# Kernel optimization log

Hardware: AMD Instinct MI355X
Metric: run time of the kernel (lower is better)

## Reference

```python
import jax, jax.numpy as jnp
import numpy as np

# Dimensions: N sites, B batch, D bond dim, d physical dim, C output classes
N, B, D, d, C = 1024, 256, 16, 2, 10
STDDEV = 1e-5
INIT_DIAG = 1.0


def setup_inputs() -> dict:
    key = jax.random.key(0)
    k1, k2, k3 = jax.random.split(key, 3)
    x = jax.random.normal(k1, (N, B, d), dtype=jnp.float32)
    eye = jnp.eye(D, dtype=jnp.float32)
    # tensor[n,:,:,i] = init_diag * I + stddev * noise  (matches TF init)
    tensor = INIT_DIAG * eye[None, :, :, None] + STDDEV * jax.random.normal(k2, (N, D, D, d), dtype=jnp.float32)
    # Aout[c] = I + stddev * noise
    Aout = eye[None, :, :] + STDDEV * jax.random.normal(k3, (C, D, D), dtype=jnp.float32)
    return {"x": x, "tensor": tensor, "Aout": Aout}


def _chain_prod(A):
    # A: (n, b, D, D) -> ordered matrix-chain product (b, D, D), log-depth tree.
    # Faithful to parallel_contract: pairwise einsum per level; odd leftover is
    # kept at the end of the list (order-preserving, associativity-equivalent).
    while A.shape[0] > 1:
        n = A.shape[0]
        half = n // 2
        prod = jnp.einsum('nblk,nbkr->nblr', A[0:2 * half:2], A[1:2 * half:2])
        if n % 2 == 1:
            prod = jnp.concatenate([prod, A[-1:]], axis=0)
        A = prod
    return A[0]


def reference(x, tensor, Aout):
    # A: (N, B, D, D) site matrices after contracting input features
    A = jnp.einsum('nbi,nlri->nblr', x, tensor)
    nhalf = A.shape[0] // 2
    # Left half product, take row 0 (left boundary); right half, take col 0
    Al = _chain_prod(A[:nhalf])[:, 0, :]   # (B, D)
    Ar = _chain_prod(A[nhalf:])[:, :, 0]   # (B, D)
    # out[b,o] = Al[b] @ Aout[o] @ Ar[b]
    return jnp.einsum('bl,olr,br->bo', Al, Aout, Ar)
```

## Files before the change

### kernel.cpp

```cpp
#include <hip/hip_runtime.h>


#define BATCH  256
#define NCLS   10
#define NSITES 1024
#define NGRP   16
#define SEGLEN 16

typedef __attribute__((ext_vector_type(8))) short short8;
typedef __attribute__((ext_vector_type(4))) float f32x4;
typedef __attribute__((ext_vector_type(4))) unsigned short us4;

static __device__ __forceinline__ unsigned short bf16tr(float f) {
    return (unsigned short)(__builtin_bit_cast(unsigned, f) >> 16);
}
static __device__ __forceinline__ unsigned short bf16rne(float f) {
    unsigned u = __builtin_bit_cast(unsigned, f);
    u += 0x7FFFu + ((u >> 16) & 1u);
    return (unsigned short)(u >> 16);
}
static __device__ __forceinline__ float bf16tof(unsigned short h) {
    return __builtin_bit_cast(float, (unsigned)h << 16);
}

__global__ __launch_bounds__(256) void ta_pack_kernel(
    const float* __restrict__ tensor, unsigned short* __restrict__ Ta)
{
    __shared__ float s[512];
    const int n = blockIdx.x, t = threadIdx.x;
    *(float2*)(s + 2 * t) = *(const float2*)(tensor + (size_t)n * 512 + 2 * t);
    __syncthreads();
    const int o0 = 2 * t, m = o0 >> 5, k0 = o0 & 31;
    const float v0 = s[(k0 & 15) * 32 + m * 2 + (k0 >> 4)];
    const int k1 = k0 + 1;
    const float v1 = s[(k1 & 15) * 32 + m * 2 + (k1 >> 4)];
    const unsigned pk = (unsigned)bf16rne(v0) | ((unsigned)bf16rne(v1) << 16);
    ((unsigned*)Ta)[(size_t)n * 256 + t] = pk;
}

__global__ __launch_bounds__(256) void chain_kernel(
    const float* __restrict__ x,
    const unsigned short* __restrict__ Ta,
    unsigned short* __restrict__ M2)
{
    __shared__ unsigned short rm[4 * 256];
    __shared__ unsigned short cm[4 * 256];
    const int t = threadIdx.x, wave = t >> 6, lane = t & 63;
    const int quad = lane >> 4, l15 = lane & 15;
    const int b = blockIdx.x >> 4, g = blockIdx.x & 15;
    const int seg = g * 4 + wave, n0 = seg * SEGLEN;

    const int qm = quad & 1;
    const int bidx0 = (32 * qm + l15) * 4;
    const int bidx1 = bidx0 + 64;

    f32x4 d;
#pragma unroll
    for (int r = 0; r < 4; ++r) d[r] = (quad * 4 + r == l15) ? 1.0f : 0.0f;

    const float2* __restrict__ xp = (const float2*)x;

#pragma unroll 4
    for (int s = 0; s < SEGLEN; ++s) {
        const int n = n0 + s;
        const float2 xv = xp[(size_t)n * BATCH + b];
        const float xs = (quad < 2) ? xv.x : xv.y;
        const short8 af = *(const short8*)(Ta + (size_t)n * 512 + l15 * 32 + quad * 8);
        float w[8];
#pragma unroll
        for (int r = 0; r < 4; ++r) {
            w[r]     = __builtin_bit_cast(float,
                        __builtin_amdgcn_ds_bpermute(bidx0, __builtin_bit_cast(int, d[r])));
            w[4 + r] = __builtin_bit_cast(float,
                        __builtin_amdgcn_ds_bpermute(bidx1, __builtin_bit_cast(int, d[r])));
        }
        short8 bf;
#pragma unroll
        for (int j = 0; j < 8; ++j) bf[j] = (short)bf16tr(xs * w[j]);
        f32x4 c = {0.0f, 0.0f, 0.0f, 0.0f};
        d = __builtin_amdgcn_mfma_f32_16x16x32_bf16(af, bf, c, 0, 0, 0);
    }

#pragma unroll
    for (int r = 0; r < 4; ++r)
        rm[wave * 256 + (quad * 4 + r) * 16 + l15] = bf16tr(d[r]);
    {
        us4 pk = {bf16tr(d[0]), bf16tr(d[1]), bf16tr(d[2]), bf16tr(d[3])};
        *(us4*)(cm + wave * 256 + l15 * 16 + quad * 4) = pk;
    }
    __syncthreads();

    const short8 z8 = {0, 0, 0, 0, 0, 0, 0, 0};

    short8 af1 = z8, bf1 = z8;
    if (wave < 2 && quad < 2) {
        af1 = *(const short8*)(rm + (2 * wave + 1) * 256 + l15 * 16 + quad * 8);
        bf1 = *(const short8*)(cm + (2 * wave) * 256 + l15 * 16 + quad * 8);
    }
    __syncthreads();
    if (wave < 2) {
        f32x4 c = {0.0f, 0.0f, 0.0f, 0.0f};
        f32x4 q = __builtin_amdgcn_mfma_f32_16x16x32_bf16(af1, bf1, c, 0, 0, 0);
#pragma unroll
        for (int r = 0; r < 4; ++r)
            rm[wave * 256 + (quad * 4 + r) * 16 + l15] = bf16tr(q[r]);
        us4 pk = {bf16tr(q[0]), bf16tr(q[1]), bf16tr(q[2]), bf16tr(q[3])};
        *(us4*)(cm + wave * 256 + l15 * 16 + quad * 4) = pk;
    }
    __syncthreads();

    if (wave == 0) {
        short8 af2 = z8, bf2 = z8;
        if (quad < 2) {
            af2 = *(const short8*)(rm + 1 * 256 + l15 * 16 + quad * 8);
            bf2 = *(const short8*)(cm + 0 * 256 + l15 * 16 + quad * 8);
        }
        f32x4 c = {0.0f, 0.0f, 0.0f, 0.0f};
        f32x4 rr = __builtin_amdgcn_mfma_f32_16x16x32_bf16(af2, bf2, c, 0, 0, 0);
        us4 pk = {bf16tr(rr[0]), bf16tr(rr[1]), bf16tr(rr[2]), bf16tr(rr[3])};
        *(us4*)(M2 + ((size_t)b * NGRP + g) * 256 + l15 * 16 + quad * 4) = pk;
    }
}

__global__ __launch_bounds__(256) void combine_kernel(
    const unsigned short* __restrict__ M2,
    const float* __restrict__ Aout,
    float* __restrict__ out)
{
    __shared__ unsigned short rm[16 * 256];
    __shared__ unsigned short cm[16 * 256];
    const int b = blockIdx.x, t = threadIdx.x;
    const int wave = t >> 6, lane = t & 63, quad = lane >> 4, l15 = lane & 15;

    const short8* __restrict__ src = (const short8*)(M2 + (size_t)b * NGRP * 256);
#pragma unroll
    for (int i2 = 0; i2 < 2; ++i2) {
        const int i = t + 256 * i2;
        const short8 v = src[i];
        *((short8*)cm + i) = v;
        const int mat = i >> 5, c = (i >> 1) & 15, r0 = (i & 1) * 8;
#pragma unroll
        for (int e = 0; e < 8; ++e)
            rm[mat * 256 + (r0 + e) * 16 + c] = (unsigned short)v[e];
    }
    __syncthreads();

    const short8 z8 = {0, 0, 0, 0, 0, 0, 0, 0};

    for (int lvl = 0; lvl < 3; ++lvl) {
        const int np = 8 >> lvl;
        short8 afr[2], bfr[2];
        int pids[2], nmine = 0;
        for (int p = wave; p < np; p += 4) {
            short8 a = z8, bb = z8;
            if (quad < 2) {
                a  = *(const short8*)(rm + (2 * p + 1) * 256 + l15 * 16 + quad * 8);
                bb = *(const short8*)(cm + (2 * p) * 256 + l15 * 16 + quad * 8);
            }
            afr[nmine] = a; bfr[nmine] = bb; pids[nmine] = p; ++nmine;
        }
        __syncthreads();
        for (int ii = 0; ii < nmine; ++ii) {
            f32x4 c = {0.0f, 0.0f, 0.0f, 0.0f};
            f32x4 r = __builtin_amdgcn_mfma_f32_16x16x32_bf16(afr[ii], bfr[ii], c, 0, 0, 0);
            const int p = pids[ii];
#pragma unroll
            for (int rr = 0; rr < 4; ++rr)
                rm[p * 256 + (quad * 4 + rr) * 16 + l15] = bf16tr(r[rr]);
            us4 pk = {bf16tr(r[0]), bf16tr(r[1]), bf16tr(r[2]), bf16tr(r[3])};
            *(us4*)(cm + p * 256 + l15 * 16 + quad * 4) = pk;
        }
        __syncthreads();
    }

    if (t < NCLS * 16) {
        const int o = t >> 4, r = t & 15;
        const float vr = bf16tof(rm[256 + r]);
        float s = 0.0f;
#pragma unroll
        for (int l = 0; l < 16; ++l)
            s = __builtin_fmaf(bf16tof(rm[l * 16]), Aout[((size_t)o * 16 + l) * 16 + r], s);
        s *= vr;
#pragma unroll
        for (int off = 8; off > 0; off >>= 1)
            s += __shfl_xor(s, off, 16);
        if (r == 0) out[(size_t)b * NCLS + o] = s;
    }
}

extern "C" void kernel_launch(void* const* d_in, const int* in_sizes, int n_in,
                              void* d_out, int out_size, void* d_ws, size_t ws_size,
                              hipStream_t stream)
{
    const float* x      = (const float*)d_in[0];
    const float* tensor = (const float*)d_in[1];
    const float* Aout   = (const float*)d_in[2];
    float* out = (float*)d_out;

    unsigned short* Ta = (unsigned short*)d_ws;
    unsigned short* M2 = (unsigned short*)((char*)d_ws + (1 << 20));

    ta_pack_kernel<<<NSITES, 256, 0, stream>>>(tensor, Ta);
    chain_kernel<<<BATCH * NGRP, 256, 0, stream>>>(x, Ta, M2);
    combine_kernel<<<BATCH, 256, 0, stream>>>(M2, Aout, out);
}
```

Before: 89.16 us.

## Fuse chain and combine kernels into one per-batch 1024-thread block

Merges the segment-chain kernel and the combine kernel into one launch, with one 1024-thread block per batch element. Each of the 16 waves now advances four independent segment chains in an interleaved loop, giving the MFMA units independent work to hide latency. The full 64-matrix tree reduction then runs in shared memory, so the M2 round trip through global memory and one launch go away. The cost is only 256 blocks, which lowers the number of blocks in flight, plus higher register pressure from four accumulators per wave and 64 KB of LDS per block.

```diff
diff --git a/kernel.cpp b/kernel.cpp
--- a/kernel.cpp
+++ b/kernel.cpp
@@ -4,8 +4,10 @@
 #define BATCH  256
 #define NCLS   10
 #define NSITES 1024
-#define NGRP   16
+#define NSEGB  64
 #define SEGLEN 16
+#define NWAVE  16
+#define CPW    4
 
 typedef __attribute__((ext_vector_type(8))) short short8;
 typedef __attribute__((ext_vector_type(4))) float f32x4;
@@ -38,120 +40,72 @@
     ((unsigned*)Ta)[(size_t)n * 256 + t] = pk;
 }
 
-__global__ __launch_bounds__(256) void chain_kernel(
+__global__ __launch_bounds__(1024) void chain_kernel(
     const float* __restrict__ x,
     const unsigned short* __restrict__ Ta,
-    unsigned short* __restrict__ M2)
+    const float* __restrict__ Aout,
+    float* __restrict__ out)
 {
-    __shared__ unsigned short rm[4 * 256];
-    __shared__ unsigned short cm[4 * 256];
+    __shared__ unsigned short rm[NSEGB * 256];
+    __shared__ unsigned short cm[NSEGB * 256];
     const int t = threadIdx.x, wave = t >> 6, lane = t & 63;
     const int quad = lane >> 4, l15 = lane & 15;
-    const int b = blockIdx.x >> 4, g = blockIdx.x & 15;
-    const int seg = g * 4 + wave, n0 = seg * SEGLEN;
+    const int b = blockIdx.x;
 
     const int qm = quad & 1;
     const int bidx0 = (32 * qm + l15) * 4;
     const int bidx1 = bidx0 + 64;
 
-    f32x4 d;
+    f32x4 d[CPW];
 #pragma unroll
-    for (int r = 0; r < 4; ++r) d[r] = (quad * 4 + r == l15) ? 1.0f : 0.0f;
+    for (int c = 0; c < CPW; ++c)
+#pragma unroll
+        for (int r = 0; r < 4; ++r) d[c][r] = (quad * 4 + r == l15) ? 1.0f : 0.0f;
 
     const float2* __restrict__ xp = (const float2*)x;
 
-#pragma unroll 4
+#pragma unroll 1
     for (int s = 0; s < SEGLEN; ++s) {
-        const int n = n0 + s;
-        const float2 xv = xp[(size_t)n * BATCH + b];
-        const float xs = (quad < 2) ? xv.x : xv.y;
-        const short8 af = *(const short8*)(Ta + (size_t)n * 512 + l15 * 32 + quad * 8);
-        float w[8];
 #pragma unroll
-        for (int r = 0; r < 4; ++r) {
-            w[r]     = __builtin_bit_cast(float,
-                        __builtin_amdgcn_ds_bpermute(bidx0, __builtin_bit_cast(int, d[r])));
-            w[4 + r] = __builtin_bit_cast(float,
-                        __builtin_amdgcn_ds_bpermute(bidx1, __builtin_bit_cast(int, d[r])));
+        for (int c = 0; c < CPW; ++c) {
+            const int n = (wave * CPW + c) * SEGLEN + s;
+            const float2 xv = xp[(size_t)n * BATCH + b];
+            const float xs = (quad < 2) ? xv.x : xv.y;
+            const short8 af = *(const short8*)(Ta + (size_t)n * 512 + l15 * 32 + quad * 8);
+            float w[8];
+#pragma unroll
+            for (int r = 0; r < 4; ++r) {
+                w[r]     = __builtin_bit_cast(float,
+                            __builtin_amdgcn_ds_bpermute(bidx0, __builtin_bit_cast(int, d[c][r])));
+                w[4 + r] = __builtin_bit_cast(float,
+                            __builtin_amdgcn_ds_bpermute(bidx1, __builtin_bit_cast(int, d[c][r])));
+            }
+            short8 bf;
+#pragma unroll
+            for (int j = 0; j < 8; ++j) bf[j] = (short)bf16tr(xs * w[j]);
+            f32x4 cz = {0.0f, 0.0f, 0.0f, 0.0f};
+            d[c] = __builtin_amdgcn_mfma_f32_16x16x32_bf16(af, bf, cz, 0, 0, 0);
         }
-        short8 bf;
-#pragma unroll
-        for (int j = 0; j < 8; ++j) bf[j] = (short)bf16tr(xs * w[j]);
-        f32x4 c = {0.0f, 0.0f, 0.0f, 0.0f};
-        d = __builtin_amdgcn_mfma_f32_16x16x32_bf16(af, bf, c, 0, 0, 0);
     }
 
 #pragma unroll
-    for (int r = 0; r < 4; ++r)
-        rm[wave * 256 + (quad * 4 + r) * 16 + l15] = bf16tr(d[r]);
-    {
-        us4 pk = {bf16tr(d[0]), bf16tr(d[1]), bf16tr(d[2]), bf16tr(d[3])};
-        *(us4*)(cm + wave * 256 + l15 * 16 + quad * 4) = pk;
+    for (int c = 0; c < CPW; ++c) {
+        const int p = wave * CPW + c;
+#pragma unroll
+        for (int r = 0; r < 4; ++r)
+            rm[p * 256 + (quad * 4 + r) * 16 + l15] = bf16tr(d[c][r]);
+        us4 pk = {bf16tr(d[c][0]), bf16tr(d[c][1]), bf16tr(d[c][2]), bf16tr(d[c][3])};
+        *(us4*)(cm + p * 256 + l15 * 16 + quad * 4) = pk;
     }
     __syncthreads();
 
     const short8 z8 = {0, 0, 0, 0, 0, 0, 0, 0};
 
-    short8 af1 = z8, bf1 = z8;
-    if (wave < 2 && quad < 2) {
-        af1 = *(const short8*)(rm + (2 * wave + 1) * 256 + l15 * 16 + quad * 8);
-        bf1 = *(const short8*)(cm + (2 * wave) * 256 + l15 * 16 + quad * 8);
-    }
-    __syncthreads();
-    if (wave < 2) {
-        f32x4 c = {0.0f, 0.0f, 0.0f, 0.0f};
-        f32x4 q = __builtin_amdgcn_mfma_f32_16x16x32_bf16(af1, bf1, c, 0, 0, 0);
-#pragma unroll
-        for (int r = 0; r < 4; ++r)
-            rm[wave * 256 + (quad * 4 + r) * 16 + l15] = bf16tr(q[r]);
-        us4 pk = {bf16tr(q[0]), bf16tr(q[1]), bf16tr(q[2]), bf16tr(q[3])};
-        *(us4*)(cm + wave * 256 + l15 * 16 + quad * 4) = pk;
-    }
-    __syncthreads();
-
-    if (wave == 0) {
-        short8 af2 = z8, bf2 = z8;
-        if (quad < 2) {
-            af2 = *(const short8*)(rm + 1 * 256 + l15 * 16 + quad * 8);
-            bf2 = *(const short8*)(cm + 0 * 256 + l15 * 16 + quad * 8);
-        }
-        f32x4 c = {0.0f, 0.0f, 0.0f, 0.0f};
-        f32x4 rr = __builtin_amdgcn_mfma_f32_16x16x32_bf16(af2, bf2, c, 0, 0, 0);
-        us4 pk = {bf16tr(rr[0]), bf16tr(rr[1]), bf16tr(rr[2]), bf16tr(rr[3])};
-        *(us4*)(M2 + ((size_t)b * NGRP + g) * 256 + l15 * 16 + quad * 4) = pk;
-    }
-}
-
-__global__ __launch_bounds__(256) void combine_kernel(
-    const unsigned short* __restrict__ M2,
-    const float* __restrict__ Aout,
-    float* __restrict__ out)
-{
-    __shared__ unsigned short rm[16 * 256];
-    __shared__ unsigned short cm[16 * 256];
-    const int b = blockIdx.x, t = threadIdx.x;
-    const int wave = t >> 6, lane = t & 63, quad = lane >> 4, l15 = lane & 15;
-
-    const short8* __restrict__ src = (const short8*)(M2 + (size_t)b * NGRP * 256);
-#pragma unroll
-    for (int i2 = 0; i2 < 2; ++i2) {
-        const int i = t + 256 * i2;
-        const short8 v = src[i];
-        *((short8*)cm + i) = v;
-        const int mat = i >> 5, c = (i >> 1) & 15, r0 = (i & 1) * 8;
-#pragma unroll
-        for (int e = 0; e < 8; ++e)
-            rm[mat * 256 + (r0 + e) * 16 + c] = (unsigned short)v[e];
-    }
-    __syncthreads();
-
-    const short8 z8 = {0, 0, 0, 0, 0, 0, 0, 0};
-
-    for (int lvl = 0; lvl < 3; ++lvl) {
-        const int np = 8 >> lvl;
+    for (int lvl = 0; lvl < 5; ++lvl) {
+        const int np = 32 >> lvl;
         short8 afr[2], bfr[2];
         int pids[2], nmine = 0;
-        for (int p = wave; p < np; p += 4) {
+        for (int p = wave; p < np; p += NWAVE) {
             short8 a = z8, bb = z8;
             if (quad < 2) {
                 a  = *(const short8*)(rm + (2 * p + 1) * 256 + l15 * 16 + quad * 8);
@@ -161,8 +115,8 @@
         }
         __syncthreads();
         for (int ii = 0; ii < nmine; ++ii) {
-            f32x4 c = {0.0f, 0.0f, 0.0f, 0.0f};
-            f32x4 r = __builtin_amdgcn_mfma_f32_16x16x32_bf16(afr[ii], bfr[ii], c, 0, 0, 0);
+            f32x4 cz = {0.0f, 0.0f, 0.0f, 0.0f};
+            f32x4 r = __builtin_amdgcn_mfma_f32_16x16x32_bf16(afr[ii], bfr[ii], cz, 0, 0, 0);
             const int p = pids[ii];
 #pragma unroll
             for (int rr = 0; rr < 4; ++rr)
@@ -198,9 +152,7 @@
     float* out = (float*)d_out;
 
     unsigned short* Ta = (unsigned short*)d_ws;
-    unsigned short* M2 = (unsigned short*)((char*)d_ws + (1 << 20));
 
     ta_pack_kernel<<<NSITES, 256, 0, stream>>>(tensor, Ta);
-    chain_kernel<<<BATCH * NGRP, 256, 0, stream>>>(x, Ta, M2);
-    combine_kernel<<<BATCH, 256, 0, stream>>>(M2, Aout, out);
+    chain_kernel<<<BATCH, 1024, 0, stream>>>(x, Ta, Aout, out);
 }
```

After: 101.8 us. 1.14x slower.
